# Optimization experiments

Hardware: AMD Instinct MI355X
Metric: run time of the kernel (lower is better)

## Reference

```python
import jax, jax.numpy as jnp
import numpy as np

K_SIZE = 5  # pred_k_size


def setup_inputs() -> dict:
    key = jax.random.key(0)
    k1, k2 = jax.random.split(key)
    bs, c, h, w = 4, 64, 160, 160
    fm = jax.random.normal(k1, (bs, c, h, w), dtype=jnp.float32)
    kernel = jax.random.normal(k2, (bs, K_SIZE * K_SIZE, h, w), dtype=jnp.float32)
    return {"fm": fm, "kernel": kernel, "dilation": 1}


def reference(fm, kernel, dilation):
    # fm: [bs, c, h, w]; kernel: [bs, k*k, h, w]
    bs, c, h, w = fm.shape
    k = K_SIZE
    pad = (k // 2) * dilation
    feat_padded = jnp.pad(fm, ((0, 0), (0, 0), (pad, pad), (pad, pad)))
    kern = jnp.flip(kernel, axis=1)  # torch.flip(kernel, dims=[1])
    # stack k*k shifted views: [bs, k*k, c, h, w]
    img_stack = jnp.stack(
        [
            feat_padded[:, :, i * dilation:i * dilation + h, j * dilation:j * dilation + w]
            for i in range(k)
            for j in range(k)
        ],
        axis=1,
    )
    # per-pixel weighted sum over the k*k taps -> [bs, c, h, w]
    res = jnp.sum(kern[:, :, None, :, :] * img_stack, axis=1)
    return res
```

## Files before the change

kernel.cpp:

```cpp
#include <hip/hip_runtime.h>

#define K    5
#define KK   25
#define H    160
#define W    160
#define C    64
#define BS   4
#define HW   (H * W)

#define TX   32
#define TY   8
#define CPB  16
#define CPW  4
#define BLK  256

#define FR   (TY + 4)
#define FS   44
#define WLS  36

__global__ __launch_bounds__(BLK) void kconv_kernel(
    const float* __restrict__ fm,
    const float* __restrict__ kern,
    const int*  __restrict__ dil,
    float* __restrict__ out)
{
    __shared__ float fmlds[CPB * FR * FS];
    __shared__ float wlds[KK * TY * WLS];

    const int tid   = threadIdx.x;
    const int x0    = blockIdx.x * TX;
    const int y0    = blockIdx.y * TY;
    const int b     = blockIdx.z >> 2;
    const int cg    = blockIdx.z & 3;
    const int cbase = cg * CPB;
    const int d     = dil[0];

    const int lane = tid & 63;
    const int qx   = lane & 7;
    const int ty   = lane >> 3;
    const int c0   = (tid >> 6) * CPW;

    if (d == 1) {
        const float* fmb = fm + ((size_t)b * C + cbase) * HW;
        for (int idx = tid; idx < CPB * FR * 10; idx += BLK) {
            const int ch  = idx / (FR * 10);
            const int rem = idx - ch * (FR * 10);
            const int r   = rem / 10;
            const int f4  = rem - r * 10;
            const int gy  = y0 - 2 + r;
            const int gx  = x0 - 4 + 4 * f4;
            float4 v = make_float4(0.f, 0.f, 0.f, 0.f);
            if (gy >= 0 && gy < H && gx >= 0 && gx < W)
                v = *(const float4*)(fmb + (size_t)ch * HW + (size_t)gy * W + gx);
            *(float4*)&fmlds[(ch * FR + r) * FS + 4 * f4] = v;
        }
        const float* kb = kern + (size_t)b * KK * HW + (size_t)y0 * W + x0;
        for (int idx = tid; idx < KK * TY * 8; idx += BLK) {
            const int m   = idx / (TY * 8);
            const int rem = idx - m * (TY * 8);
            const int r   = rem / 8;
            const int f4  = rem - r * 8;
            const float4 v = *(const float4*)(kb + (size_t)m * HW + (size_t)r * W + 4 * f4);
            *(float4*)&wlds[((KK - 1 - m) * TY + r) * WLS + 4 * f4] = v;
        }
        __syncthreads();

        float acc[CPW][4];
#pragma unroll
        for (int c = 0; c < CPW; ++c)
#pragma unroll
            for (int p = 0; p < 4; ++p) acc[c][p] = 0.f;

#pragma unroll
        for (int i = 0; i < K; ++i) {
            float wr[K][4];
#pragma unroll
            for (int j = 0; j < K; ++j) {
                const float4 wv = *(const float4*)&wlds[((i * K + j) * TY + ty) * WLS + 4 * qx];
                wr[j][0] = wv.x; wr[j][1] = wv.y; wr[j][2] = wv.z; wr[j][3] = wv.w;
            }
            float win[CPW][8];
#pragma unroll
            for (int c = 0; c < CPW; ++c) {
                const int base = ((c0 + c) * FR + ty + i) * FS + 4 * qx + 2;
#pragma unroll
                for (int k = 0; k < 4; ++k) {
                    const float2 t = *(const float2*)&fmlds[base + 2 * k];
                    win[c][2 * k]     = t.x;
                    win[c][2 * k + 1] = t.y;
                }
            }
#pragma unroll
            for (int c = 0; c < CPW; ++c)
#pragma unroll
                for (int j = 0; j < K; ++j)
#pragma unroll
                    for (int p = 0; p < 4; ++p)
                        acc[c][p] = fmaf(wr[j][p], win[c][p + j], acc[c][p]);
        }

        float* ob = out + ((size_t)b * C + cbase + c0) * HW + (size_t)(y0 + ty) * W + x0 + 4 * qx;
#pragma unroll
        for (int c = 0; c < CPW; ++c) {
            const float4 o = {acc[c][0], acc[c][1], acc[c][2], acc[c][3]};
            *(float4*)(ob + (size_t)c * HW) = o;
        }
    } else {
        const int x = x0 + 4 * qx;
        const int y = y0 + ty;
        const float* fb  = fm  + ((size_t)b * C + cbase + c0) * HW;
        float*       ob  = out + ((size_t)b * C + cbase + c0) * HW + (size_t)y * W + x;
        const float* kbp = kern + (size_t)b * KK * HW + (size_t)y * W + x;
#pragma unroll 1
        for (int p = 0; p < 4; ++p) {
            const int xx = x + p;
            float wgt[KK];
            int   offs[KK];
#pragma unroll 1
            for (int i = 0; i < K; ++i) {
                const int  yy  = y + (i - 2) * d;
                const bool yok = (yy >= 0) && (yy < H);
                const int  yc  = min(max(yy, 0), H - 1);
#pragma unroll 1
                for (int j = 0; j < K; ++j) {
                    const int  xc  = xx + (j - 2) * d;
                    const bool ok  = yok && (xc >= 0) && (xc < W);
                    const int  xcc = min(max(xc, 0), W - 1);
                    const int  t   = i * K + j;
                    wgt[t]  = ok ? kbp[(size_t)(KK - 1 - t) * HW + p] : 0.f;
                    offs[t] = yc * W + xcc;
                }
            }
#pragma unroll 1
            for (int c = 0; c < CPW; ++c) {
                const float* fc = fb + (size_t)c * HW;
                float a2 = 0.f;
#pragma unroll 1
                for (int t = 0; t < KK; ++t) a2 = fmaf(wgt[t], fc[offs[t]], a2);
                ob[(size_t)c * HW + p] = a2;
            }
        }
    }
}

extern "C" void kernel_launch(void* const* d_in, const int* in_sizes, int n_in,
                              void* d_out, int out_size, void* d_ws, size_t ws_size,
                              hipStream_t stream)
{
    const float* fm   = (const float*)d_in[0];
    const float* kern = (const float*)d_in[1];
    const int*   dil  = (const int*)d_in[2];
    float*       out  = (float*)d_out;

    dim3 grid(W / TX, H / TY, BS * (C / CPB));
    kconv_kernel<<<grid, dim3(BLK), 0, stream>>>(fm, kern, dil, out);
}
```

Baseline: 115.8 us.

## Load per-pixel weights directly from global memory instead of staging in LDS

Removes the shared-memory staging buffer for the per-pixel 25-tap weights. Each thread now reads its float4 of weights straight from global memory inside the tap loop. The feature tile row stride changes from 44 to 46 and is written as two float2 stores to reduce LDS bank conflicts. This cuts LDS footprint, which may raise occupancy, and drops a staging pass. In exchange, the four warps of a block that share the same weights each issue their own global loads, relying on cache hits.

```diff
diff --git a/kernel.cpp b/kernel.cpp
--- a/kernel.cpp
+++ b/kernel.cpp
@@ -15,8 +15,7 @@
 #define BLK  256
 
 #define FR   (TY + 4)
-#define FS   44
-#define WLS  36
+#define FS   46
 
 __global__ __launch_bounds__(BLK) void kconv_kernel(
     const float* __restrict__ fm,
@@ -25,7 +24,6 @@
     float* __restrict__ out)
 {
     __shared__ float fmlds[CPB * FR * FS];
-    __shared__ float wlds[KK * TY * WLS];
 
     const int tid   = threadIdx.x;
     const int x0    = blockIdx.x * TX;
@@ -40,6 +38,10 @@
     const int ty   = lane >> 3;
     const int c0   = (tid >> 6) * CPW;
 
+    const int x = x0 + 4 * qx;
+    const int y = y0 + ty;
+    const float* kb = kern + (size_t)b * KK * HW + (size_t)y * W + x;
+
     if (d == 1) {
         const float* fmb = fm + ((size_t)b * C + cbase) * HW;
         for (int idx = tid; idx < CPB * FR * 10; idx += BLK) {
@@ -52,16 +54,9 @@
             float4 v = make_float4(0.f, 0.f, 0.f, 0.f);
             if (gy >= 0 && gy < H && gx >= 0 && gx < W)
                 v = *(const float4*)(fmb + (size_t)ch * HW + (size_t)gy * W + gx);
-            *(float4*)&fmlds[(ch * FR + r) * FS + 4 * f4] = v;
-        }
-        const float* kb = kern + (size_t)b * KK * HW + (size_t)y0 * W + x0;
-        for (int idx = tid; idx < KK * TY * 8; idx += BLK) {
-            const int m   = idx / (TY * 8);
-            const int rem = idx - m * (TY * 8);
-            const int r   = rem / 8;
-            const int f4  = rem - r * 8;
-            const float4 v = *(const float4*)(kb + (size_t)m * HW + (size_t)r * W + 4 * f4);
-            *(float4*)&wlds[((KK - 1 - m) * TY + r) * WLS + 4 * f4] = v;
+            float* dst = &fmlds[(ch * FR + r) * FS + 4 * f4];
+            *(float2*)dst       = make_float2(v.x, v.y);
+            *(float2*)(dst + 2) = make_float2(v.z, v.w);
         }
         __syncthreads();
 
@@ -76,7 +71,8 @@
             float wr[K][4];
 #pragma unroll
             for (int j = 0; j < K; ++j) {
-                const float4 wv = *(const float4*)&wlds[((i * K + j) * TY + ty) * WLS + 4 * qx];
+                const int t = i * K + j;
+                const float4 wv = *(const float4*)(kb + (size_t)(KK - 1 - t) * HW);
                 wr[j][0] = wv.x; wr[j][1] = wv.y; wr[j][2] = wv.z; wr[j][3] = wv.w;
             }
             float win[CPW][8];
@@ -85,9 +81,9 @@
                 const int base = ((c0 + c) * FR + ty + i) * FS + 4 * qx + 2;
 #pragma unroll
                 for (int k = 0; k < 4; ++k) {
-                    const float2 t = *(const float2*)&fmlds[base + 2 * k];
-                    win[c][2 * k]     = t.x;
-                    win[c][2 * k + 1] = t.y;
+                    const float2 t2 = *(const float2*)&fmlds[base + 2 * k];
+                    win[c][2 * k]     = t2.x;
+                    win[c][2 * k + 1] = t2.y;
                 }
             }
 #pragma unroll
@@ -99,18 +95,15 @@
                         acc[c][p] = fmaf(wr[j][p], win[c][p + j], acc[c][p]);
         }
 
-        float* ob = out + ((size_t)b * C + cbase + c0) * HW + (size_t)(y0 + ty) * W + x0 + 4 * qx;
+        float* ob = out + ((size_t)b * C + cbase + c0) * HW + (size_t)y * W + x;
 #pragma unroll
         for (int c = 0; c < CPW; ++c) {
             const float4 o = {acc[c][0], acc[c][1], acc[c][2], acc[c][3]};
             *(float4*)(ob + (size_t)c * HW) = o;
         }
     } else {
-        const int x = x0 + 4 * qx;
-        const int y = y0 + ty;
-        const float* fb  = fm  + ((size_t)b * C + cbase + c0) * HW;
-        float*       ob  = out + ((size_t)b * C + cbase + c0) * HW + (size_t)y * W + x;
-        const float* kbp = kern + (size_t)b * KK * HW + (size_t)y * W + x;
+        const float* fb = fm  + ((size_t)b * C + cbase + c0) * HW;
+        float*       ob = out + ((size_t)b * C + cbase + c0) * HW + (size_t)y * W + x;
 #pragma unroll 1
         for (int p = 0; p < 4; ++p) {
             const int xx = x + p;
@@ -127,7 +120,7 @@
                     const bool ok  = yok && (xc >= 0) && (xc < W);
                     const int  xcc = min(max(xc, 0), W - 1);
                     const int  t   = i * K + j;
-                    wgt[t]  = ok ? kbp[(size_t)(KK - 1 - t) * HW + p] : 0.f;
+                    wgt[t]  = ok ? kb[(size_t)(KK - 1 - t) * HW + p] : 0.f;
                     offs[t] = yc * W + xcc;
                 }
             }
```

Result: faster. 103.5 us (-10.6%).
